# Performance work log

Measured on AMD Instinct MI355X. Metric: run time of the kernel, lower is better.

Reference implementation:

```python
import jax, jax.numpy as jnp
import numpy as np

B, T, C, HS = 8, 2048, 1024, 64


def setup_inputs() -> dict:
    key = jax.random.key(0)
    ks = jax.random.split(key, 4)
    x = jax.random.normal(ks[0], (B, T, C), dtype=jnp.float32)
    Wq = jax.random.normal(ks[1], (C, HS), dtype=jnp.float32) * (C ** -0.5)
    Wk = jax.random.normal(ks[2], (C, HS), dtype=jnp.float32) * (C ** -0.5)
    Wv = jax.random.normal(ks[3], (C, HS), dtype=jnp.float32) * (C ** -0.5)
    mask = jnp.tril(jnp.ones((T, T), dtype=jnp.int32))  # causal mask
    return {"x": x, "mask": mask, "Wq": Wq, "Wk": Wk, "Wv": Wv}


def reference(x, mask, Wq, Wk, Wv):
    # x: [B,T,C]; bias-free projections to head_size
    q = jnp.einsum("btc,ch->bth", x, Wq)
    k = jnp.einsum("btc,ch->bth", x, Wk)
    v = jnp.einsum("btc,ch->bth", x, Wv)
    # NOTE: original scales by C**-0.5 (n_embd), not head_size**-0.5
    wei = jnp.einsum("bth,bsh->bts", q, k) * (x.shape[-1] ** -0.5)
    wei = jnp.where(mask[None, :, :] == 0, -jnp.inf, wei)
    wei = jax.nn.softmax(wei, axis=-1)
    # dropout is identity in eval / p=0
    out = jnp.einsum("bts,bsh->bth", wei, v)
    return out
```

## Files before the change

### kernel.cpp

```cpp
#include <hip/hip_runtime.h>
#include <hip/hip_bf16.h>


#define B_  8
#define T_  2048
#define C_  1024
#define HS_ 64
#define MROWS (B_ * T_)

typedef __attribute__((ext_vector_type(8))) short bf16x8;
typedef __attribute__((ext_vector_type(4))) float f32x4;
typedef __attribute__((ext_vector_type(4))) float float4v;

#define SCALE_LOG2 0.04508422037445829f

__device__ __forceinline__ short f2bs(float f) {
    __hip_bfloat16 h = __float2bfloat16(f);
    short s;
    __builtin_memcpy(&s, &h, 2);
    return s;
}

__global__ __launch_bounds__(256) void wt_kernel(
    const float* __restrict__ Wq,
    const float* __restrict__ Wk,
    const float* __restrict__ Wv,
    __hip_bfloat16* __restrict__ Wt) {
    __shared__ float tile[64][65];
    const int m  = blockIdx.x >> 4;
    const int r0 = (blockIdx.x & 15) * 64;
    const float* W = (m == 0) ? Wq : (m == 1) ? Wk : Wv;
    const int i = threadIdx.x >> 6;
    const int j = threadIdx.x & 63;
#pragma unroll
    for (int p = 0; p < 16; ++p) {
        int r = p * 4 + i;
        tile[r][j] = W[(size_t)(r0 + r) * HS_ + j];
    }
    __syncthreads();
#pragma unroll
    for (int p = 0; p < 16; ++p) {
        int h = p * 4 + i;
        Wt[(size_t)m * (HS_ * C_) + (size_t)h * C_ + r0 + j] =
            __float2bfloat16(tile[j][h]);
    }
}

__global__ __launch_bounds__(256, 2) void proj_kernel(
    const float* __restrict__ x,
    const __hip_bfloat16* __restrict__ Wt,
    __hip_bfloat16* __restrict__ Q,
    __hip_bfloat16* __restrict__ Kp,
    __hip_bfloat16* __restrict__ Vt)
{
    __shared__ float xt0[32 * 64];
    __shared__ float xt1[32 * 64];

    const int lane = threadIdx.x & 63;
    const int wave = threadIdx.x >> 6;
    const int quad = lane >> 4;
    const int l15  = lane & 15;
    const int row0 = blockIdx.x * 32;

    const int u16  = lane & 15;
    const int rsub = lane >> 4;
    const float* gsrc[2];
#pragma unroll
    for (int h = 0; h < 2; ++h) {
        int rl = wave * 8 + h * 4 + rsub;
        gsrc[h] = x + (size_t)(row0 + rl) * C_ + ((u16 ^ (rl & 7)) << 2);
    }

    const __hip_bfloat16* wbase[3];
#pragma unroll
    for (int j = 0; j < 3; ++j) {
        int nt = wave * 3 + j;
        int h  = ((nt & 3) * 16) + l15;
        wbase[j] = Wt + (size_t)(nt >> 2) * (HS_ * C_) + (size_t)h * C_ + quad * 8;
    }

    f32x4 acc[2][3];
#pragma unroll
    for (int rt = 0; rt < 2; ++rt)
#pragma unroll
        for (int j = 0; j < 3; ++j)
            acc[rt][j] = (f32x4){0.f, 0.f, 0.f, 0.f};

    bf16x8 bfr0[2][3], bfr1[2][3];

#define ISSUE_DMA(XT, kc)                                                    \
    do {                                                                     \
        _Pragma("unroll")                                                    \
        for (int hh = 0; hh < 2; ++hh)                                       \
            __builtin_amdgcn_global_load_lds(                                \
                (const __attribute__((address_space(1))) unsigned*)          \
                    (gsrc[hh] + (kc)),                                       \
                (__attribute__((address_space(3))) unsigned*)                \
                    (&XT[(wave * 8 + hh * 4) * 64]),                         \
                16, 0, 0);                                                   \
    } while (0)

#define LOAD_B(BF, kc)                                                       \
    do {                                                                     \
        _Pragma("unroll")                                                    \
        for (int ks = 0; ks < 2; ++ks)                                       \
            _Pragma("unroll")                                                \
            for (int j = 0; j < 3; ++j)                                      \
                BF[ks][j] = *(const bf16x8*)(wbase[j] + (kc) + ks * 32);     \
    } while (0)

#define COMPUTE(XT, BF)                                                      \
    do {                                                                     \
        _Pragma("unroll")                                                    \
        for (int ks = 0; ks < 2; ++ks) {                                     \
            bf16x8 a[2];                                                     \
            _Pragma("unroll")                                                \
            for (int rt = 0; rt < 2; ++rt) {                                 \
                const float4v* bp =                                          \
                    (const float4v*)&XT[(rt * 16 + l15) * 64];               \
                const int sw_ = l15 & 7;                                     \
                float4v f0 = bp[(ks * 8 + quad * 2) ^ sw_];                  \
                float4v f1 = bp[(ks * 8 + quad * 2 + 1) ^ sw_];              \
                _Pragma("unroll")                                            \
                for (int e = 0; e < 4; ++e) {                                \
                    a[rt][e]     = f2bs(f0[e]);                              \
                    a[rt][4 + e] = f2bs(f1[e]);                              \
                }                                                            \
            }                                                                \
            _Pragma("unroll")                                                \
            for (int rt = 0; rt < 2; ++rt)                                   \
                _Pragma("unroll")                                            \
                for (int j = 0; j < 3; ++j)                                  \
                    acc[rt][j] = __builtin_amdgcn_mfma_f32_16x16x32_bf16(    \
                        a[rt], BF[ks][j], acc[rt][j], 0, 0, 0);              \
        }                                                                    \
    } while (0)

    ISSUE_DMA(xt0, 0);
    LOAD_B(bfr0, 0);

#pragma unroll 1
    for (int kc = 0; kc < C_; kc += 128) {
        __syncthreads();
        if (kc + 64 < C_) {
            ISSUE_DMA(xt1, kc + 64);
            LOAD_B(bfr1, kc + 64);
        }
        COMPUTE(xt0, bfr0);
        __syncthreads();
        if (kc + 128 < C_) {
            ISSUE_DMA(xt0, kc + 128);
            LOAD_B(bfr0, kc + 128);
        }
        COMPUTE(xt1, bfr1);
    }
#undef ISSUE_DMA
#undef LOAD_B
#undef COMPUTE

#pragma unroll
    for (int rt = 0; rt < 2; ++rt) {
#pragma unroll
        for (int j = 0; j < 3; ++j) {
            int nt  = wave * 3 + j;
            int mtx = nt >> 2;
            int col = (nt & 3) * 16 + l15;
#pragma unroll
            for (int r = 0; r < 4; ++r) {
                int row = row0 + rt * 16 + quad * 4 + r;
                float av = acc[rt][j][r];
                if (mtx == 0) {
                    Q[(size_t)row * HS_ + col] =
                        __float2bfloat16(av * SCALE_LOG2);
                } else if (mtx == 1) {
                    Kp[(size_t)row * HS_ + col] = __float2bfloat16(av);
                } else {
                    int bidx = row >> 11;
                    int t    = row & 2047;
                    Vt[((size_t)bidx * HS_ + col) * T_ + t] =
                        __float2bfloat16(av);
                }
            }
        }
    }
}

__global__ __launch_bounds__(256, 2) void attn_kernel(
    const __hip_bfloat16* __restrict__ Q,
    const __hip_bfloat16* __restrict__ Kp,
    const __hip_bfloat16* __restrict__ Vt,
    float* __restrict__ out)
{
    __shared__ __align__(16) __hip_bfloat16 plds[4][32 * 72];
    __shared__ float o_lds[4][32][65];
    __shared__ float l_lds[4][32][17];

    const int tid  = threadIdx.x;
    const int wv   = tid >> 6;
    const int lane = tid & 63;
    const int quad = lane >> 4;
    const int l15  = lane & 15;
    const int b    = blockIdx.x & 7;
    const int idx  = blockIdx.x >> 3;
    const int lt   = (idx < 32) ? (63 - idx) : (idx - 32);
    const int qb   = lt * 32;
    const int rowg = b * T_ + qb;

    bf16x8 qf[2][2];
#pragma unroll
    for (int rt = 0; rt < 2; ++rt)
#pragma unroll
        for (int h = 0; h < 2; ++h)
            qf[rt][h] = *(const bf16x8*)
                (Q + (size_t)(rowg + rt * 16 + l15) * HS_ + h * 32 + quad * 8);

    f32x4 o[2][4];
#pragma unroll
    for (int rt = 0; rt < 2; ++rt)
#pragma unroll
        for (int j = 0; j < 4; ++j) o[rt][j] = (f32x4){0.f, 0.f, 0.f, 0.f};
    float lp[2][4] = {{0.f,0.f,0.f,0.f},{0.f,0.f,0.f,0.f}};

    __hip_bfloat16* pb = plds[wv];
    const int nt = (qb + 31) / 64 + 1;

#define LOADK(KF, kb_)                                                       \
    do {                                                                     \
        const __hip_bfloat16* Kb_ = Kp + (size_t)(b * T_ + (kb_)) * HS_;     \
        _Pragma("unroll")                                                    \
        for (int c = 0; c < 4; ++c)                                          \
            _Pragma("unroll")                                                \
            for (int h = 0; h < 2; ++h)                                      \
                KF[c][h] = *(const bf16x8*)                                  \
                    (Kb_ + (size_t)(c * 16 + l15) * HS_ + h * 32 + quad * 8);\
    } while (0)

#define PROC(KF, kb_)                                                        \
    do {                                                                     \
        bf16x8 vf[2][4];                                                     \
        _Pragma("unroll")                                                    \
        for (int h = 0; h < 2; ++h)                                          \
            _Pragma("unroll")                                                \
            for (int j = 0; j < 4; ++j)                                      \
                vf[h][j] = *(const bf16x8*)                                  \
                    (Vt + ((size_t)b * HS_ + j * 16 + l15) * T_ +            \
                     (kb_) + h * 32 + quad * 8);                             \
        f32x4 s[2][4];                                                       \
        _Pragma("unroll")                                                    \
        for (int rt = 0; rt < 2; ++rt)                                       \
            _Pragma("unroll")                                                \
            for (int c = 0; c < 4; ++c) {                                    \
                s[rt][c] = (f32x4){0.f, 0.f, 0.f, 0.f};                      \
                s[rt][c] = __builtin_amdgcn_mfma_f32_16x16x32_bf16(          \
                    qf[rt][0], KF[c][0], s[rt][c], 0, 0, 0);                 \
                s[rt][c] = __builtin_amdgcn_mfma_f32_16x16x32_bf16(          \
                    qf[rt][1], KF[c][1], s[rt][c], 0, 0, 0);                 \
            }                                                                \
        const bool msk = ((kb_) + 63 > qb);                                  \
        _Pragma("unroll")                                                    \
        for (int rt = 0; rt < 2; ++rt)                                       \
            _Pragma("unroll")                                                \
            for (int c = 0; c < 4; ++c)                                      \
                _Pragma("unroll")                                            \
                for (int r = 0; r < 4; ++r) {                                \
                    float pv = __builtin_amdgcn_exp2f(s[rt][c][r]);          \
                    if (msk) {                                               \
                        int row = qb + rt * 16 + quad * 4 + r;               \
                        if ((kb_) + c * 16 + l15 > row) pv = 0.f;            \
                    }                                                        \
                    lp[rt][r] += pv;                                         \
                    pb[(rt * 16 + quad * 4 + r) * 72 + c * 16 + l15] =       \
                        __float2bfloat16(pv);                                \
                }                                                            \
        asm volatile("s_waitcnt lgkmcnt(0)" ::: "memory");                   \
        _Pragma("unroll")                                                    \
        for (int rt = 0; rt < 2; ++rt) {                                     \
            bf16x8 pf0 = *(const bf16x8*)                                    \
                (pb + (rt * 16 + l15) * 72 + quad * 8);                      \
            bf16x8 pf1 = *(const bf16x8*)                                    \
                (pb + (rt * 16 + l15) * 72 + 32 + quad * 8);                 \
            _Pragma("unroll")                                                \
            for (int j = 0; j < 4; ++j) {                                    \
                o[rt][j] = __builtin_amdgcn_mfma_f32_16x16x32_bf16(          \
                    pf0, vf[0][j], o[rt][j], 0, 0, 0);                       \
                o[rt][j] = __builtin_amdgcn_mfma_f32_16x16x32_bf16(          \
                    pf1, vf[1][j], o[rt][j], 0, 0, 0);                       \
            }                                                                \
        }                                                                    \
    } while (0)

    bf16x8 kA[4][2], kB[4][2];
    if (wv < nt) LOADK(kA, wv * 64);
    int i = 0;
#pragma unroll 1
    for (; wv + 4 * (i + 1) < nt; i += 2) {
        LOADK(kB, (wv + 4 * (i + 1)) * 64);
        PROC(kA, (wv + 4 * i) * 64);
        if (wv + 4 * (i + 2) < nt) LOADK(kA, (wv + 4 * (i + 2)) * 64);
        PROC(kB, (wv + 4 * (i + 1)) * 64);
    }
    if (wv + 4 * i < nt) PROC(kA, (wv + 4 * i) * 64);
#undef LOADK
#undef PROC

#pragma unroll
    for (int rt = 0; rt < 2; ++rt) {
#pragma unroll
        for (int j = 0; j < 4; ++j)
#pragma unroll
            for (int r = 0; r < 4; ++r)
                o_lds[wv][rt * 16 + quad * 4 + r][j * 16 + l15] = o[rt][j][r];
#pragma unroll
        for (int r = 0; r < 4; ++r)
            l_lds[wv][rt * 16 + quad * 4 + r][l15] = lp[rt][r];
    }
    __syncthreads();

    if (tid < 32) {
        float s = 0.f;
#pragma unroll
        for (int w = 0; w < 4; ++w)
            for (int c = 0; c < 16; ++c) s += l_lds[w][tid][c];
        l_lds[0][tid][0] = 1.0f / s;
    }
    __syncthreads();

    const int h = tid & 63;
#pragma unroll
    for (int k = 0; k < 8; ++k) {
        int row = (tid >> 6) * 8 + k;
        float s = o_lds[0][row][h] + o_lds[1][row][h] +
                  o_lds[2][row][h] + o_lds[3][row][h];
        out[(size_t)(rowg + row) * HS_ + h] = s * l_lds[0][row][0];
    }
}

extern "C" void kernel_launch(void* const* d_in, const int* in_sizes, int n_in,
                              void* d_out, int out_size, void* d_ws, size_t ws_size,
                              hipStream_t stream) {
    (void)in_sizes; (void)n_in; (void)out_size; (void)ws_size;
    const float* x  = (const float*)d_in[0];
    const float* Wq = (const float*)d_in[2];
    const float* Wk = (const float*)d_in[3];
    const float* Wv = (const float*)d_in[4];

    __hip_bfloat16* ws = (__hip_bfloat16*)d_ws;
    __hip_bfloat16* Wt = ws;
    __hip_bfloat16* Q  = ws + 196608;
    __hip_bfloat16* Kp = ws + 196608 + 1048576;
    __hip_bfloat16* Vt = ws + 196608 + 2 * 1048576;

    wt_kernel<<<48, 256, 0, stream>>>(Wq, Wk, Wv, Wt);
    proj_kernel<<<MROWS / 32, 256, 0, stream>>>(x, Wt, Q, Kp, Vt);
    attn_kernel<<<(T_ / 32) * B_, 256, 0, stream>>>(Q, Kp, Vt, (float*)d_out);
}
```

Measured before the change: 145.6 us.

## Drop K double-buffering and alias LDS buffers to raise attention occupancy

```diff
diff --git a/kernel.cpp b/kernel.cpp
--- a/kernel.cpp
+++ b/kernel.cpp
@@ -185,15 +185,16 @@
     }
 }
 
-__global__ __launch_bounds__(256, 2) void attn_kernel(
+__global__ __launch_bounds__(256, 3) void attn_kernel(
     const __hip_bfloat16* __restrict__ Q,
     const __hip_bfloat16* __restrict__ Kp,
     const __hip_bfloat16* __restrict__ Vt,
     float* __restrict__ out)
 {
-    __shared__ __align__(16) __hip_bfloat16 plds[4][32 * 72];
-    __shared__ float o_lds[4][32][65];
-    __shared__ float l_lds[4][32][17];
+    __shared__ __align__(16) char smem[33280 + 8704];
+    __hip_bfloat16* plds = (__hip_bfloat16*)smem;
+    float (*o_lds)[32][65] = (float (*)[32][65])smem;
+    float (*l_lds)[32][17] = (float (*)[32][17])(smem + 33280);
 
     const int tid  = threadIdx.x;
     const int wv   = tid >> 6;
@@ -221,29 +222,28 @@
         for (int j = 0; j < 4; ++j) o[rt][j] = (f32x4){0.f, 0.f, 0.f, 0.f};
     float lp[2][4] = {{0.f,0.f,0.f,0.f},{0.f,0.f,0.f,0.f}};
 
-    __hip_bfloat16* pb = plds[wv];
+    __hip_bfloat16* pb = plds + wv * 2304;
     const int nt = (qb + 31) / 64 + 1;
-
-#define LOADK(KF, kb_)                                                       \
+    const __hip_bfloat16* Kbase = Kp + (size_t)b * T_ * HS_;
+    const __hip_bfloat16* Vbase = Vt + (size_t)b * HS_ * T_;
+
+#define PROC(kb_)                                                            \
     do {                                                                     \
-        const __hip_bfloat16* Kb_ = Kp + (size_t)(b * T_ + (kb_)) * HS_;     \
+        bf16x8 kf[4][2];                                                     \
+        const __hip_bfloat16* Kb_ = Kbase + (size_t)(kb_) * HS_;             \
         _Pragma("unroll")                                                    \
         for (int c = 0; c < 4; ++c)                                          \
             _Pragma("unroll")                                                \
             for (int h = 0; h < 2; ++h)                                      \
-                KF[c][h] = *(const bf16x8*)                                  \
+                kf[c][h] = *(const bf16x8*)                                  \
                     (Kb_ + (size_t)(c * 16 + l15) * HS_ + h * 32 + quad * 8);\
-    } while (0)
-
-#define PROC(KF, kb_)                                                        \
-    do {                                                                     \
         bf16x8 vf[2][4];                                                     \
         _Pragma("unroll")                                                    \
         for (int h = 0; h < 2; ++h)                                          \
             _Pragma("unroll")                                                \
             for (int j = 0; j < 4; ++j)                                      \
                 vf[h][j] = *(const bf16x8*)                                  \
-                    (Vt + ((size_t)b * HS_ + j * 16 + l15) * T_ +            \
+                    (Vbase + (size_t)(j * 16 + l15) * T_ +                   \
                      (kb_) + h * 32 + quad * 8);                             \
         f32x4 s[2][4];                                                       \
         _Pragma("unroll")                                                    \
@@ -252,9 +252,9 @@
             for (int c = 0; c < 4; ++c) {                                    \
                 s[rt][c] = (f32x4){0.f, 0.f, 0.f, 0.f};                      \
                 s[rt][c] = __builtin_amdgcn_mfma_f32_16x16x32_bf16(          \
-                    qf[rt][0], KF[c][0], s[rt][c], 0, 0, 0);                 \
+                    qf[rt][0], kf[c][0], s[rt][c], 0, 0, 0);                 \
                 s[rt][c] = __builtin_amdgcn_mfma_f32_16x16x32_bf16(          \
-                    qf[rt][1], KF[c][1], s[rt][c], 0, 0, 0);                 \
+                    qf[rt][1], kf[c][1], s[rt][c], 0, 0, 0);                 \
             }                                                                \
         const bool msk = ((kb_) + 63 > qb);                                  \
         _Pragma("unroll")                                                    \
@@ -289,19 +289,11 @@
         }                                                                    \
     } while (0)
 
-    bf16x8 kA[4][2], kB[4][2];
-    if (wv < nt) LOADK(kA, wv * 64);
-    int i = 0;
 #pragma unroll 1
-    for (; wv + 4 * (i + 1) < nt; i += 2) {
-        LOADK(kB, (wv + 4 * (i + 1)) * 64);
-        PROC(kA, (wv + 4 * i) * 64);
-        if (wv + 4 * (i + 2) < nt) LOADK(kA, (wv + 4 * (i + 2)) * 64);
-        PROC(kB, (wv + 4 * (i + 1)) * 64);
-    }
-    if (wv + 4 * i < nt) PROC(kA, (wv + 4 * i) * 64);
-#undef LOADK
+    for (int i = wv; i < nt; i += 4) PROC(i * 64);
 #undef PROC
+
+    __syncthreads();
 
 #pragma unroll
     for (int rt = 0; rt < 2; ++rt) {
```

After: 147.9 us. No clear change (+1.6%).
